# Kernel tuning notes

Hardware: AMD Instinct MI355X
Metric: run time of the kernel (lower is better)

## Reference

```python
import jax, jax.numpy as jnp
import numpy as np

N, E, D_IN, D_H, D_OUT = 100000, 1600000, 64, 64, 64


def _lin_params(key, d_out, d_in):
    k1, k2 = jax.random.split(key)
    s = 1.0 / np.sqrt(d_in)
    W = jax.random.uniform(k1, (d_out, d_in), jnp.float32, -s, s)
    b = jax.random.uniform(k2, (d_out,), jnp.float32, -s, s)
    return W, b


def setup_inputs() -> dict:
    key = jax.random.key(0)
    ks = jax.random.split(key, 10)
    x = jax.random.normal(ks[0], (N, D_IN), jnp.float32)
    edge_index = jax.random.randint(ks[1], (2, E), 0, N, jnp.int64)
    Wq1, bq1 = _lin_params(ks[2], D_H, D_IN)
    Wk1, bk1 = _lin_params(ks[3], D_H, D_IN)
    Wv1, bv1 = _lin_params(ks[4], D_H, D_IN)
    Ws1, bs1 = _lin_params(ks[5], D_H, D_IN)
    Wq2, bq2 = _lin_params(ks[6], D_OUT, D_H)
    Wk2, bk2 = _lin_params(ks[7], D_OUT, D_H)
    Wv2, bv2 = _lin_params(ks[8], D_OUT, D_H)
    Ws2, bs2 = _lin_params(ks[9], D_OUT, D_H)
    return dict(x=x, edge_index=edge_index,
                Wq1=Wq1, bq1=bq1, Wk1=Wk1, bk1=bk1, Wv1=Wv1, bv1=bv1, Ws1=Ws1, bs1=bs1,
                Wq2=Wq2, bq2=bq2, Wk2=Wk2, bk2=bk2, Wv2=Wv2, bv2=bv2, Ws2=Ws2, bs2=bs2)


def transformer_conv(x, src, dst, Wq, bq, Wk, bk, Wv, bv, Ws, bs):
    # PyG TransformerConv, heads=1, concat=True, root_weight=True, no edge_attr.
    n = x.shape[0]
    q = x @ Wq.T + bq                       # [N, C] query of target nodes
    k = x @ Wk.T + bk                       # [N, C] key of source nodes
    v = x @ Wv.T + bv                       # [N, C] value of source nodes
    scale = 1.0 / np.sqrt(q.shape[-1])
    score = jnp.sum(q[dst] * k[src], axis=-1) * scale   # [E]
    # segment softmax over incoming edges of each target node
    m = jax.lax.stop_gradient(jax.ops.segment_max(score, dst, num_segments=n))
    e = jnp.exp(score - m[dst])                          # [E]
    denom = jax.ops.segment_sum(e, dst, num_segments=n)  # [N]
    alpha = e / denom[dst]                               # [E]
    out = jax.ops.segment_sum(alpha[:, None] * v[src], dst, num_segments=n)  # [N, C]
    return out + (x @ Ws.T + bs)            # root/skip connection


def reference(x, edge_index,
              Wq1, bq1, Wk1, bk1, Wv1, bv1, Ws1, bs1,
              Wq2, bq2, Wk2, bk2, Wv2, bv2, Ws2, bs2):
    src, dst = edge_index[0], edge_index[1]
    h = transformer_conv(x, src, dst, Wq1, bq1, Wk1, bk1, Wv1, bv1, Ws1, bs1)
    h = jax.nn.relu(h)
    # dropout is identity in eval/reference mode
    h = transformer_conv(h, src, dst, Wq2, bq2, Wk2, bk2, Wv2, bv2, Ws2, bs2)
    return h
```

## Files before the change

kernel.cpp:

```cpp
#include <hip/hip_runtime.h>
#include <math.h>

#define DCH 64

typedef __attribute__((ext_vector_type(8))) short short8v;
typedef __attribute__((ext_vector_type(4))) float f32x4;

__device__ __forceinline__ unsigned short f2bf(float f) {
    unsigned u = __builtin_bit_cast(unsigned, f);
    unsigned r = u + 0x7FFF + ((u >> 16) & 1);
    return (unsigned short)(r >> 16);
}


__global__ void zero_kernel(int* __restrict__ p, int n) {
    int i = blockIdx.x * blockDim.x + threadIdx.x;
    if (i < n) p[i] = 0;
}

__global__ void hist_kernel(const int* __restrict__ ei, int* __restrict__ cnt, int E) {
    int stride = gridDim.x * blockDim.x;
    for (int e = blockIdx.x * blockDim.x + threadIdx.x; e < E; e += stride) {
        int d = ei[(size_t)E + e];
        atomicAdd(&cnt[d], 1);
    }
}

__global__ void scan1_kernel(const int* __restrict__ cnt, int* __restrict__ offs,
                             int* __restrict__ partial, int n) {
    __shared__ int sh[1024];
    int i = blockIdx.x * 1024 + threadIdx.x;
    int val = (i < n) ? cnt[i] : 0;
    sh[threadIdx.x] = val;
    __syncthreads();
    for (int d = 1; d < 1024; d <<= 1) {
        int t = (threadIdx.x >= d) ? sh[threadIdx.x - d] : 0;
        __syncthreads();
        sh[threadIdx.x] += t;
        __syncthreads();
    }
    if (i < n) offs[i] = sh[threadIdx.x] - val;
    if (threadIdx.x == 1023) partial[blockIdx.x] = sh[1023];
}

__global__ void scan2_kernel(int* __restrict__ partial, int* __restrict__ total, int nb) {
    __shared__ int sh[1024];
    int val = (threadIdx.x < nb) ? partial[threadIdx.x] : 0;
    sh[threadIdx.x] = val;
    __syncthreads();
    for (int d = 1; d < 1024; d <<= 1) {
        int t = (threadIdx.x >= d) ? sh[threadIdx.x - d] : 0;
        __syncthreads();
        sh[threadIdx.x] += t;
        __syncthreads();
    }
    if (threadIdx.x < nb) partial[threadIdx.x] = sh[threadIdx.x] - val;
    if (threadIdx.x == 1023) *total = sh[1023];
}

__global__ void scan3_kernel(int* __restrict__ offs, const int* __restrict__ partial, int n) {
    int i = blockIdx.x * 1024 + threadIdx.x;
    if (i < n) offs[i] += partial[blockIdx.x];
}

__global__ void scatter_kernel(const int* __restrict__ ei, const int* __restrict__ offs,
                               int* __restrict__ fill, int* __restrict__ ssrc, int E) {
    int stride = gridDim.x * blockDim.x;
    for (int e = blockIdx.x * blockDim.x + threadIdx.x; e < E; e += stride) {
        int s = ei[e];
        int d = ei[(size_t)E + e];
        int pos = offs[d] + atomicAdd(&fill[d], 1);
        ssrc[pos] = s;
    }
}


__global__ __launch_bounds__(256, 3)
void linear4_kernel(const float* __restrict__ x,
                    const float* __restrict__ Wq, const float* __restrict__ bq,
                    const float* __restrict__ Wk, const float* __restrict__ bk,
                    const float* __restrict__ Wv, const float* __restrict__ bv,
                    const float* __restrict__ Ws, const float* __restrict__ bs,
                    float* __restrict__ oq, float* __restrict__ ok,
                    float* __restrict__ ov, float* __restrict__ os,
                    int n) {
    const int tid = threadIdx.x;
    const int w = tid >> 6;
    const int lane = tid & 63;
    const int l16 = lane & 15;
    const int lhi = lane >> 4;
    const float* W; const float* b; float* o;
    if (w == 0)      { W = Wq; b = bq; o = oq; }
    else if (w == 1) { W = Wk; b = bk; o = ok; }
    else if (w == 2) { W = Wv; b = bv; o = ov; }
    else             { W = Ws; b = bs; o = os; }
    const int base = blockIdx.x * 64;

    short8v Bf[4][2];
    #pragma unroll
    for (int nt = 0; nt < 4; ++nt) {
        const float* wrow = W + (size_t)(nt * 16 + l16) * DCH;
        #pragma unroll
        for (int ks = 0; ks < 2; ++ks) {
            const float4* wp = (const float4*)(wrow + ks * 32 + lhi * 8);
            float4 lo = wp[0], hi = wp[1];
            short8v f;
            f[0] = (short)f2bf(lo.x); f[1] = (short)f2bf(lo.y);
            f[2] = (short)f2bf(lo.z); f[3] = (short)f2bf(lo.w);
            f[4] = (short)f2bf(hi.x); f[5] = (short)f2bf(hi.y);
            f[6] = (short)f2bf(hi.z); f[7] = (short)f2bf(hi.w);
            Bf[nt][ks] = f;
        }
    }
    float bv4[4];
    #pragma unroll
    for (int nt = 0; nt < 4; ++nt) bv4[nt] = b[nt * 16 + l16];

    f32x4 acc[4][4];
    #pragma unroll
    for (int mt = 0; mt < 4; ++mt)
        #pragma unroll
        for (int nt = 0; nt < 4; ++nt)
            acc[mt][nt] = (f32x4)0.f;

    #pragma unroll
    for (int mt = 0; mt < 4; ++mt) {
        int row = base + mt * 16 + l16;
        if (row > n - 1) row = n - 1;
        const float* xp = x + (size_t)row * DCH + lhi * 8;
        float4 a0 = *(const float4*)xp;
        float4 a1 = *(const float4*)(xp + 4);
        float4 a2 = *(const float4*)(xp + 32);
        float4 a3 = *(const float4*)(xp + 36);
        short8v A0, A1;
        A0[0] = (short)f2bf(a0.x); A0[1] = (short)f2bf(a0.y);
        A0[2] = (short)f2bf(a0.z); A0[3] = (short)f2bf(a0.w);
        A0[4] = (short)f2bf(a1.x); A0[5] = (short)f2bf(a1.y);
        A0[6] = (short)f2bf(a1.z); A0[7] = (short)f2bf(a1.w);
        A1[0] = (short)f2bf(a2.x); A1[1] = (short)f2bf(a2.y);
        A1[2] = (short)f2bf(a2.z); A1[3] = (short)f2bf(a2.w);
        A1[4] = (short)f2bf(a3.x); A1[5] = (short)f2bf(a3.y);
        A1[6] = (short)f2bf(a3.z); A1[7] = (short)f2bf(a3.w);
        #pragma unroll
        for (int nt = 0; nt < 4; ++nt) {
            acc[mt][nt] = __builtin_amdgcn_mfma_f32_16x16x32_bf16(
                A0, Bf[nt][0], acc[mt][nt], 0, 0, 0);
            acc[mt][nt] = __builtin_amdgcn_mfma_f32_16x16x32_bf16(
                A1, Bf[nt][1], acc[mt][nt], 0, 0, 0);
        }
    }

    #pragma unroll
    for (int mt = 0; mt < 4; ++mt) {
        #pragma unroll
        for (int r = 0; r < 4; ++r) {
            int row = base + mt * 16 + lhi * 4 + r;
            if (row < n) {
                #pragma unroll
                for (int nt = 0; nt < 4; ++nt)
                    o[(size_t)row * DCH + nt * 16 + l16] = acc[mt][nt][r] + bv4[nt];
            }
        }
    }
}


__global__ void attn_kernel(const float* __restrict__ q, const float* __restrict__ k,
                            const float* __restrict__ v,
                            const int* __restrict__ offs, const int* __restrict__ ssrc,
                            float* __restrict__ io, int n, int do_relu) {
    const int tid = threadIdx.x;
    const int lane = tid & 63;
    const int g = lane >> 4;
    const int gl = lane & 15;
    int node = blockIdx.x * (blockDim.x >> 6) + (tid >> 6);
    if (node >= n) return;
    int e0 = offs[node], e1 = offs[node + 1];
    float4 qv = *(const float4*)&q[(size_t)node * DCH + gl * 4];
    float m = -INFINITY, den = 0.f;
    float nx = 0.f, ny = 0.f, nz = 0.f, nw = 0.f;
    for (int e = e0 + g; e < e1; e += 4) {
        int src = ssrc[e];
        float4 kv = *(const float4*)&k[(size_t)src * DCH + gl * 4];
        float dot = qv.x*kv.x + qv.y*kv.y + qv.z*kv.z + qv.w*kv.w;
        dot += __shfl_xor(dot, 1);
        dot += __shfl_xor(dot, 2);
        dot += __shfl_xor(dot, 4);
        dot += __shfl_xor(dot, 8);
        float s = dot * 0.125f;
        float mn = fmaxf(m, s);
        float c = __expf(m - mn);
        float p = __expf(s - mn);
        float4 vv = *(const float4*)&v[(size_t)src * DCH + gl * 4];
        nx = nx * c + p * vv.x;
        ny = ny * c + p * vv.y;
        nz = nz * c + p * vv.z;
        nw = nw * c + p * vv.w;
        den = den * c + p;
        m = mn;
    }
    #pragma unroll
    for (int delta = 16; delta <= 32; delta <<= 1) {
        float mo   = __shfl_xor(m, delta);
        float deno = __shfl_xor(den, delta);
        float nxo  = __shfl_xor(nx, delta);
        float nyo  = __shfl_xor(ny, delta);
        float nzo  = __shfl_xor(nz, delta);
        float nwo  = __shfl_xor(nw, delta);
        float mn = fmaxf(m, mo);
        float c  = (den  > 0.f) ? __expf(m  - mn) : 0.f;
        float co = (deno > 0.f) ? __expf(mo - mn) : 0.f;
        nx = nx * c + nxo * co;
        ny = ny * c + nyo * co;
        nz = nz * c + nzo * co;
        nw = nw * c + nwo * co;
        den = den * c + deno * co;
        m = mn;
    }
    float4 skv = *(const float4*)&io[(size_t)node * DCH + gl * 4];
    float inv = (den > 0.f) ? 1.f / den : 0.f;
    float4 o;
    o.x = nx * inv + skv.x;
    o.y = ny * inv + skv.y;
    o.z = nz * inv + skv.z;
    o.w = nw * inv + skv.w;
    if (do_relu) {
        o.x = fmaxf(o.x, 0.f); o.y = fmaxf(o.y, 0.f);
        o.z = fmaxf(o.z, 0.f); o.w = fmaxf(o.w, 0.f);
    }
    if (lane < 16) *(float4*)&io[(size_t)node * DCH + gl * 4] = o;
}


extern "C" void kernel_launch(void* const* d_in, const int* in_sizes, int n_in,
                              void* d_out, int out_size, void* d_ws, size_t ws_size,
                              hipStream_t stream) {
    const float* x   = (const float*)d_in[0];
    const int*   ei  = (const int*)d_in[1];
    const float* Wq1 = (const float*)d_in[2];  const float* bq1 = (const float*)d_in[3];
    const float* Wk1 = (const float*)d_in[4];  const float* bk1 = (const float*)d_in[5];
    const float* Wv1 = (const float*)d_in[6];  const float* bv1 = (const float*)d_in[7];
    const float* Ws1 = (const float*)d_in[8];  const float* bs1 = (const float*)d_in[9];
    const float* Wq2 = (const float*)d_in[10]; const float* bq2 = (const float*)d_in[11];
    const float* Wk2 = (const float*)d_in[12]; const float* bk2 = (const float*)d_in[13];
    const float* Wv2 = (const float*)d_in[14]; const float* bv2 = (const float*)d_in[15];
    const float* Ws2 = (const float*)d_in[16]; const float* bs2 = (const float*)d_in[17];
    int N = in_sizes[0] / DCH;
    int E = in_sizes[1] / 2;

    char* p = (char*)d_ws;
    auto alloc = [&](size_t bytes) -> void* {
        void* r = (void*)p; p += (bytes + 255) & ~(size_t)255; return r;
    };
    float* q    = (float*)alloc((size_t)N * DCH * 4);
    float* kbuf = (float*)alloc((size_t)N * DCH * 4);
    float* vbuf = (float*)alloc((size_t)N * DCH * 4);
    float* h    = (float*)alloc((size_t)N * DCH * 4);
    int* cnt  = (int*)alloc((size_t)N * 4);
    int* fill = (int*)alloc((size_t)N * 4);
    int* offs = (int*)alloc((size_t)(N + 1) * 4);
    int* part = (int*)alloc(1024 * 4);
    int* ssrc = (int*)alloc((size_t)E * 4);
    float* outp = (float*)d_out;

    int nb = (N + 1023) / 1024;

    hipLaunchKernelGGL(zero_kernel, dim3((N + 255) / 256), dim3(256), 0, stream, cnt, N);
    hipLaunchKernelGGL(zero_kernel, dim3((N + 255) / 256), dim3(256), 0, stream, fill, N);
    hipLaunchKernelGGL(hist_kernel, dim3(1024), dim3(256), 0, stream, ei, cnt, E);
    hipLaunchKernelGGL(scan1_kernel, dim3(nb), dim3(1024), 0, stream, cnt, offs, part, N);
    hipLaunchKernelGGL(scan2_kernel, dim3(1), dim3(1024), 0, stream, part, offs + N, nb);
    hipLaunchKernelGGL(scan3_kernel, dim3(nb), dim3(1024), 0, stream, offs, part, N);
    hipLaunchKernelGGL(scatter_kernel, dim3(1024), dim3(256), 0, stream, ei, offs, fill, ssrc, E);

    hipLaunchKernelGGL(linear4_kernel, dim3((N + 63) / 64), dim3(256), 0, stream,
                       x, Wq1, bq1, Wk1, bk1, Wv1, bv1, Ws1, bs1,
                       q, kbuf, vbuf, h, N);
    hipLaunchKernelGGL(attn_kernel, dim3((N + 3) / 4), dim3(256), 0, stream,
                       q, kbuf, vbuf, offs, ssrc, h, N, 1);

    hipLaunchKernelGGL(linear4_kernel, dim3((N + 63) / 64), dim3(256), 0, stream,
                       h, Wq2, bq2, Wk2, bk2, Wv2, bv2, Ws2, bs2,
                       q, kbuf, vbuf, outp, N);
    hipLaunchKernelGGL(attn_kernel, dim3((N + 3) / 4), dim3(256), 0, stream,
                       q, kbuf, vbuf, offs, ssrc, outp, N, 0);
}
```

Before: 600.9 us.

## Store K/V in bf16 and fold scatter fill counter into offsets

The linear kernel now writes K and V as packed bf16, permuting output channels so each lane stores two adjacent channels per 32-bit word. The attention kernel reads them as uint2 and unpacks, halving the gather bytes for the random per-edge K/V loads. Separately, the scatter step atomically increments offs directly, so offs ends up holding segment ends and the attention kernel reads bounds shifted by one. This drops the fill buffer and its zeroing launch. The cost is bf16 rounding of K and V values, which adds numerical error to the attention scores and outputs.

```diff
diff --git a/kernel.cpp b/kernel.cpp
--- a/kernel.cpp
+++ b/kernel.cpp
@@ -10,6 +10,12 @@
     unsigned u = __builtin_bit_cast(unsigned, f);
     unsigned r = u + 0x7FFF + ((u >> 16) & 1);
     return (unsigned short)(r >> 16);
+}
+__device__ __forceinline__ float bflo(unsigned u) {
+    return __builtin_bit_cast(float, u << 16);
+}
+__device__ __forceinline__ float bfhi(unsigned u) {
+    return __builtin_bit_cast(float, u & 0xFFFF0000u);
 }
 
 
@@ -63,13 +69,13 @@
     if (i < n) offs[i] += partial[blockIdx.x];
 }
 
-__global__ void scatter_kernel(const int* __restrict__ ei, const int* __restrict__ offs,
-                               int* __restrict__ fill, int* __restrict__ ssrc, int E) {
+__global__ void scatter_kernel(const int* __restrict__ ei, int* __restrict__ offs,
+                               int* __restrict__ ssrc, int E) {
     int stride = gridDim.x * blockDim.x;
     for (int e = blockIdx.x * blockDim.x + threadIdx.x; e < E; e += stride) {
         int s = ei[e];
         int d = ei[(size_t)E + e];
-        int pos = offs[d] + atomicAdd(&fill[d], 1);
+        int pos = atomicAdd(&offs[d], 1);
         ssrc[pos] = s;
     }
 }
@@ -81,25 +87,31 @@
                     const float* __restrict__ Wk, const float* __restrict__ bk,
                     const float* __restrict__ Wv, const float* __restrict__ bv,
                     const float* __restrict__ Ws, const float* __restrict__ bs,
-                    float* __restrict__ oq, float* __restrict__ ok,
-                    float* __restrict__ ov, float* __restrict__ os,
+                    float* __restrict__ oq, unsigned short* __restrict__ ok,
+                    unsigned short* __restrict__ ov, float* __restrict__ os,
                     int n) {
     const int tid = threadIdx.x;
     const int w = tid >> 6;
     const int lane = tid & 63;
     const int l16 = lane & 15;
     const int lhi = lane >> 4;
-    const float* W; const float* b; float* o;
-    if (w == 0)      { W = Wq; b = bq; o = oq; }
-    else if (w == 1) { W = Wk; b = bk; o = ok; }
-    else if (w == 2) { W = Wv; b = bv; o = ov; }
-    else             { W = Ws; b = bs; o = os; }
+    const bool isbf = (w == 1) || (w == 2);
+    const float* W; const float* b;
+    if (w == 0)      { W = Wq; b = bq; }
+    else if (w == 1) { W = Wk; b = bk; }
+    else if (w == 2) { W = Wv; b = bv; }
+    else             { W = Ws; b = bs; }
     const int base = blockIdx.x * 64;
 
+    int ch[4];
+    #pragma unroll
+    for (int nt = 0; nt < 4; ++nt)
+        ch[nt] = isbf ? (2 * l16 + (nt & 1) + 32 * (nt >> 1)) : (nt * 16 + l16);
+
     short8v Bf[4][2];
     #pragma unroll
     for (int nt = 0; nt < 4; ++nt) {
-        const float* wrow = W + (size_t)(nt * 16 + l16) * DCH;
+        const float* wrow = W + (size_t)ch[nt] * DCH;
         #pragma unroll
         for (int ks = 0; ks < 2; ++ks) {
             const float4* wp = (const float4*)(wrow + ks * 32 + lhi * 8);
@@ -114,7 +126,7 @@
     }
     float bv4[4];
     #pragma unroll
-    for (int nt = 0; nt < 4; ++nt) bv4[nt] = b[nt * 16 + l16];
+    for (int nt = 0; nt < 4; ++nt) bv4[nt] = b[ch[nt]];
 
     f32x4 acc[4][4];
     #pragma unroll
@@ -150,23 +162,45 @@
         }
     }
 
-    #pragma unroll
-    for (int mt = 0; mt < 4; ++mt) {
-        #pragma unroll
-        for (int r = 0; r < 4; ++r) {
-            int row = base + mt * 16 + lhi * 4 + r;
-            if (row < n) {
-                #pragma unroll
-                for (int nt = 0; nt < 4; ++nt)
-                    o[(size_t)row * DCH + nt * 16 + l16] = acc[mt][nt][r] + bv4[nt];
+    if (isbf) {
+        unsigned short* o = (w == 1) ? ok : ov;
+        #pragma unroll
+        for (int mt = 0; mt < 4; ++mt) {
+            #pragma unroll
+            for (int r = 0; r < 4; ++r) {
+                int row = base + mt * 16 + lhi * 4 + r;
+                if (row < n) {
+                    unsigned p0 = (unsigned)f2bf(acc[mt][0][r] + bv4[0])
+                                | ((unsigned)f2bf(acc[mt][1][r] + bv4[1]) << 16);
+                    unsigned p1 = (unsigned)f2bf(acc[mt][2][r] + bv4[2])
+                                | ((unsigned)f2bf(acc[mt][3][r] + bv4[3]) << 16);
+                    unsigned short* rp = o + (size_t)row * DCH;
+                    *(unsigned*)(rp + 2 * l16)      = p0;
+                    *(unsigned*)(rp + 32 + 2 * l16) = p1;
+                }
             }
         }
-    }
-}
-
-
-__global__ void attn_kernel(const float* __restrict__ q, const float* __restrict__ k,
-                            const float* __restrict__ v,
+    } else {
+        float* o = (w == 0) ? oq : os;
+        #pragma unroll
+        for (int mt = 0; mt < 4; ++mt) {
+            #pragma unroll
+            for (int r = 0; r < 4; ++r) {
+                int row = base + mt * 16 + lhi * 4 + r;
+                if (row < n) {
+                    #pragma unroll
+                    for (int nt = 0; nt < 4; ++nt)
+                        o[(size_t)row * DCH + nt * 16 + l16] = acc[mt][nt][r] + bv4[nt];
+                }
+            }
+        }
+    }
+}
+
+
+__global__ void attn_kernel(const float* __restrict__ q,
+                            const unsigned short* __restrict__ k,
+                            const unsigned short* __restrict__ v,
                             const int* __restrict__ offs, const int* __restrict__ ssrc,
                             float* __restrict__ io, int n, int do_relu) {
     const int tid = threadIdx.x;
@@ -175,14 +209,16 @@
     const int gl = lane & 15;
     int node = blockIdx.x * (blockDim.x >> 6) + (tid >> 6);
     if (node >= n) return;
-    int e0 = offs[node], e1 = offs[node + 1];
+    int e0 = (node > 0) ? offs[node - 1] : 0;
+    int e1 = offs[node];
     float4 qv = *(const float4*)&q[(size_t)node * DCH + gl * 4];
     float m = -INFINITY, den = 0.f;
     float nx = 0.f, ny = 0.f, nz = 0.f, nw = 0.f;
     for (int e = e0 + g; e < e1; e += 4) {
         int src = ssrc[e];
-        float4 kv = *(const float4*)&k[(size_t)src * DCH + gl * 4];
-        float dot = qv.x*kv.x + qv.y*kv.y + qv.z*kv.z + qv.w*kv.w;
+        uint2 kk = *(const uint2*)(k + (size_t)src * DCH + gl * 4);
+        float dot = qv.x * bflo(kk.x) + qv.y * bfhi(kk.x)
+                  + qv.z * bflo(kk.y) + qv.w * bfhi(kk.y);
         dot += __shfl_xor(dot, 1);
         dot += __shfl_xor(dot, 2);
         dot += __shfl_xor(dot, 4);
@@ -191,11 +227,11 @@
         float mn = fmaxf(m, s);
         float c = __expf(m - mn);
         float p = __expf(s - mn);
-        float4 vv = *(const float4*)&v[(size_t)src * DCH + gl * 4];
-        nx = nx * c + p * vv.x;
-        ny = ny * c + p * vv.y;
-        nz = nz * c + p * vv.z;
-        nw = nw * c + p * vv.w;
+        uint2 vv = *(const uint2*)(v + (size_t)src * DCH + gl * 4);
+        nx = nx * c + p * bflo(vv.x);
+        ny = ny * c + p * bfhi(vv.x);
+        nz = nz * c + p * bflo(vv.y);
+        nw = nw * c + p * bfhi(vv.y);
         den = den * c + p;
         m = mn;
     }
@@ -252,12 +288,11 @@
     auto alloc = [&](size_t bytes) -> void* {
         void* r = (void*)p; p += (bytes + 255) & ~(size_t)255; return r;
     };
-    float* q    = (float*)alloc((size_t)N * DCH * 4);
-    float* kbuf = (float*)alloc((size_t)N * DCH * 4);
-    float* vbuf = (float*)alloc((size_t)N * DCH * 4);
-    float* h    = (float*)alloc((size_t)N * DCH * 4);
+    float*          q    = (float*)alloc((size_t)N * DCH * 4);
+    unsigned short* kbuf = (unsigned short*)alloc((size_t)N * DCH * 2);
+    unsigned short* vbuf = (unsigned short*)alloc((size_t)N * DCH * 2);
+    float*          h    = (float*)alloc((size_t)N * DCH * 4);
     int* cnt  = (int*)alloc((size_t)N * 4);
-    int* fill = (int*)alloc((size_t)N * 4);
     int* offs = (int*)alloc((size_t)(N + 1) * 4);
     int* part = (int*)alloc(1024 * 4);
     int* ssrc = (int*)alloc((size_t)E * 4);
@@ -266,12 +301,11 @@
     int nb = (N + 1023) / 1024;
 
     hipLaunchKernelGGL(zero_kernel, dim3((N + 255) / 256), dim3(256), 0, stream, cnt, N);
-    hipLaunchKernelGGL(zero_kernel, dim3((N + 255) / 256), dim3(256), 0, stream, fill, N);
     hipLaunchKernelGGL(hist_kernel, dim3(1024), dim3(256), 0, stream, ei, cnt, E);
     hipLaunchKernelGGL(scan1_kernel, dim3(nb), dim3(1024), 0, stream, cnt, offs, part, N);
     hipLaunchKernelGGL(scan2_kernel, dim3(1), dim3(1024), 0, stream, part, offs + N, nb);
     hipLaunchKernelGGL(scan3_kernel, dim3(nb), dim3(1024), 0, stream, offs, part, N);
-    hipLaunchKernelGGL(scatter_kernel, dim3(1024), dim3(256), 0, stream, ei, offs, fill, ssrc, E);
+    hipLaunchKernelGGL(scatter_kernel, dim3(1024), dim3(256), 0, stream, ei, offs, ssrc, E);
 
     hipLaunchKernelGGL(linear4_kernel, dim3((N + 63) / 64), dim3(256), 0, stream,
                        x, Wq1, bq1, Wk1, bk1, Wv1, bv1, Ws1, bs1,
```

Result: faster. 548.7 us (-8.7%).
